# Kernel optimization log

Hardware: AMD Instinct MI355X
Metric: run time of the kernel (lower is better)

The kernel has to match this reference:

```python
import jax, jax.numpy as jnp
import numpy as np

HIDDEN = 1024
BATCH = 32
SEQ = 2048


def setup_inputs() -> dict:
    key = jax.random.key(0)
    k1, k2, k3, k4 = jax.random.split(key, 4)
    decoder_state = jax.random.normal(k1, (BATCH, HIDDEN), dtype=jnp.float32)
    encoder_outputs = jax.random.normal(k2, (BATCH, SEQ, HIDDEN), dtype=jnp.float32)
    # nn.Linear(hidden, hidden, bias=False): y = x @ W.T; store weight as (out, in)
    W = jax.random.normal(k3, (HIDDEN, HIDDEN), dtype=jnp.float32) / np.sqrt(HIDDEN)
    v = jax.random.normal(k4, (1, HIDDEN), dtype=jnp.float32) / np.sqrt(HIDDEN)
    return {"decoder_state": decoder_state, "encoder_outputs": encoder_outputs, "W": W, "v": v}


def reference(decoder_state, encoder_outputs, W, v):
    # projected encoder states: [b, s, h]
    proj = jnp.einsum('bsh,oh->bso', encoder_outputs, W)
    # additive score: tanh(proj + dec) @ v -> [b, s]
    scores = jnp.einsum('bsh,h->bs', jnp.tanh(proj + decoder_state[:, None, :]), v[0])
    weights = jax.nn.softmax(scores, axis=-1)  # [b, s]
    context = jnp.einsum('bs,bsh->bh', weights, encoder_outputs)  # [b, h]
    return (context, weights)
```

## Files before the change

### kernel.cpp

```cpp
#include <hip/hip_runtime.h>
#include <hip/hip_bf16.h>
#include <math.h>

#define HIDDEN 1024
#define BATCH 32
#define SEQ 2048
#define MTOT (BATCH * SEQ)
#define N_PLANES 8

#define BM 128
#define BN 256
#define BK 32
#define NKS (HIDDEN / BK)

typedef __attribute__((ext_vector_type(8))) short          bf16x8;
typedef __attribute__((ext_vector_type(8))) unsigned short ushort8;
typedef __attribute__((ext_vector_type(4))) float          f32x4;

#define GLOAD_LDS16(g, l) __builtin_amdgcn_global_load_lds( \
    (const __attribute__((address_space(1))) void*)(g),      \
    (__attribute__((address_space(3))) void*)(l), 16, 0, 0)

#define BARRIER() asm volatile("s_barrier" ::: "memory")
#define WAITL0()  asm volatile("s_waitcnt lgkmcnt(0)" ::: "memory")
#define WAITL6()  asm volatile("s_waitcnt lgkmcnt(6)" ::: "memory")
#define WAITV4()  asm volatile("s_waitcnt vmcnt(4)" ::: "memory")
#define WAITV8()  asm volatile("s_waitcnt vmcnt(8)" ::: "memory")
#define WAITV0()  asm volatile("s_waitcnt vmcnt(0)" ::: "memory")
#define SCHED0()  __builtin_amdgcn_sched_barrier(0)

__device__ __forceinline__ float fast_tanh(float x) {
    float e = __builtin_amdgcn_exp2f(x * 2.8853900817779268f);
    return 1.0f - 2.0f * __builtin_amdgcn_rcpf(1.0f + e);
}

__device__ __forceinline__ ushort8 cvt8(float4 lo, float4 hi) {
    float va[8] = {lo.x, lo.y, lo.z, lo.w, hi.x, hi.y, hi.z, hi.w};
    ushort8 r;
    #pragma unroll
    for (int j = 0; j < 8; ++j) {
        unsigned u = __float_as_uint(va[j]);
        r[j] = (unsigned short)((u + 0x7FFFu + ((u >> 16) & 1u)) >> 16);
    }
    return r;
}

__global__ __launch_bounds__(256) void convert_w_k(
    const float* __restrict__ W, unsigned short* __restrict__ Wb)
{
    const int i = blockIdx.x * blockDim.x + threadIdx.x;
    float4 a = ((const float4*)W)[(size_t)i * 2];
    float4 b = ((const float4*)W)[(size_t)i * 2 + 1];
    *(ushort8*)&Wb[(size_t)i * 8] = cvt8(a, b);
}

template <bool PARTIALS>
__global__ __launch_bounds__(256, 2) void score_gemm_mfma(
    const float* __restrict__ enc,
    const unsigned short* __restrict__ Wb,
    const float* __restrict__ dec,
    const float* __restrict__ v,
    float* __restrict__ outp)
{
    __shared__ unsigned short As[3][BM][BK];
    __shared__ unsigned short Bs[3][BN][BK];

    const int bid  = blockIdx.x;
    const int xcd  = bid & 7;
    const int slot = bid >> 3;
    const int mt   = xcd * 64 + (slot >> 2);
    const int nt   = slot & 3;
    const int m0   = mt * BM;
    const int n0   = nt * BN;

    const int tid  = threadIdx.x;
    const int wid  = tid >> 6;
    const int lane = tid & 63;
    const int wm   = (wid >> 1) * 64;
    const int wn   = (wid & 1) * 128;

    const int rowb = (lane & 15) * 64;
    const int swzb = (((lane >> 4) ^ (lane & 3)) * 16);

    const int chA0  = wid * 64 + lane;
    const int chA1  = 256 + wid * 64 + lane;
    const int rowA0 = chA0 >> 2, rowA1 = chA1 >> 2;
    const float* encA0 = &enc[(size_t)(m0 + rowA0) * HIDDEN
                              + (((chA0 & 3) ^ (rowA0 & 3)) * 8)];
    const float* encA1 = &enc[(size_t)(m0 + rowA1) * HIDDEN
                              + (((chA1 & 3) ^ (rowA1 & 3)) * 8)];

    auto loadA = [&](int k0, float4& l0, float4& h0, float4& l1, float4& h1) {
        l0 = *(const float4*)(encA0 + k0);
        h0 = *(const float4*)(encA0 + k0 + 4);
        l1 = *(const float4*)(encA1 + k0);
        h1 = *(const float4*)(encA1 + k0 + 4);
    };
    auto writeA = [&](int buf, float4 l0, float4 h0, float4 l1, float4 h1) {
        *(ushort8*)((char*)&As[buf][0][0] + (size_t)chA0 * 16) = cvt8(l0, h0);
        *(ushort8*)((char*)&As[buf][0][0] + (size_t)chA1 * 16) = cvt8(l1, h1);
    };
    auto stageB = [&](int buf, int k0) {
        #pragma unroll
        for (int c = 0; c < 4; ++c) {
            const int chw = c * 256 + wid * 64;
            const int ch  = chw + lane;
            const int row = ch >> 2;
            const int gk  = k0 + (((ch & 3) ^ (row & 3)) * 8);
            GLOAD_LDS16(&Wb[(size_t)(n0 + row) * HIDDEN + gk],
                        (char*)&Bs[buf][0][0] + (size_t)chw * 16);
        }
    };

    {
        float4 p0l0, p0h0, p0l1, p0h1, p1l0, p1h0, p1l1, p1h1;
        loadA(0, p0l0, p0h0, p0l1, p0h1);
        stageB(0, 0);
        loadA(BK, p1l0, p1h0, p1l1, p1h1);
        stageB(1, BK);
        asm volatile("s_waitcnt vmcnt(12)" ::: "memory"); SCHED0();
        writeA(0, p0l0, p0h0, p0l1, p0h1);
        WAITV4(); SCHED0();
        writeA(1, p1l0, p1h0, p1l1, p1h1);
        WAITL0(); SCHED0();
        BARRIER();
    }

    f32x4 acc[4][8] = {};
    float4 al0, ah0, al1, ah1;

    #pragma unroll 1
    for (int t = 0; t < NKS; ++t) {
        const int cur  = t % 3;
        const int nxt  = (t + 2) % 3;
        const int prv  = (t + 1) % 3;
        const bool more = (t + 2 < NKS);
        const int knxt = (t + 2) * BK;
        const char* Ab = (const char*)&As[cur][0][0];
        const char* Bb = (const char*)&Bs[cur][0][0];

        bf16x8 af[4], bf[8];

        #pragma unroll
        for (int fi = 0; fi < 4; ++fi)
            af[fi] = *(const bf16x8*)(Ab + (wm + fi * 16) * 64 + rowb + swzb);
        #pragma unroll
        for (int fj = 0; fj < 8; ++fj)
            bf[fj] = *(const bf16x8*)(Bb + (wn + fj * 16) * 64 + rowb + swzb);
        SCHED0();

        if (t >= 1 && t + 1 < NKS) {
            WAITV4(); SCHED0();
            writeA(prv, al0, ah0, al1, ah1);
            SCHED0();
        }
        if (more) {
            loadA(knxt, al0, ah0, al1, ah1);
            SCHED0();
            stageB(nxt, knxt);
            SCHED0();
        }

        WAITL6(); SCHED0();
        __builtin_amdgcn_s_setprio(1);
        #pragma unroll
        for (int fi = 0; fi < 4; ++fi)
            #pragma unroll
            for (int fj = 0; fj < 4; ++fj)
                acc[fi][fj] = __builtin_amdgcn_mfma_f32_16x16x32_bf16(
                    af[fi], bf[fj], acc[fi][fj], 0, 0, 0);
        __builtin_amdgcn_s_setprio(0);
        SCHED0();

        WAITL0(); SCHED0();
        __builtin_amdgcn_s_setprio(1);
        #pragma unroll
        for (int fi = 0; fi < 4; ++fi)
            #pragma unroll
            for (int fj = 4; fj < 8; ++fj)
                acc[fi][fj] = __builtin_amdgcn_mfma_f32_16x16x32_bf16(
                    af[fi], bf[fj], acc[fi][fj], 0, 0, 0);
        __builtin_amdgcn_s_setprio(0);
        SCHED0();

        if (more)             { WAITV8(); }
        else if (t + 1 < NKS) { WAITV0(); }
        SCHED0();
        if (t + 1 < NKS) BARRIER();
    }

    const int rowgrp = lane >> 4;
    const int col    = lane & 15;
    const int b      = m0 >> 11;
    const float* decb = dec + (size_t)b * HIDDEN;

    float2 dv[8];
    #pragma unroll
    for (int fj = 0; fj < 8; ++fj) {
        const int n = n0 + wn + fj * 16 + col;
        dv[fj] = make_float2(decb[n], v[n]);
    }

    const size_t plane = (size_t)(nt * 2 + (wid & 1)) * MTOT;

    #pragma unroll
    for (int fi = 0; fi < 4; ++fi) {
        #pragma unroll
        for (int r = 0; r < 4; ++r) {
            const int m = m0 + wm + fi * 16 + rowgrp * 4 + r;
            float rp = 0.f;
            #pragma unroll
            for (int fj = 0; fj < 8; ++fj)
                rp = fmaf(fast_tanh(acc[fi][fj][r] + dv[fj].x), dv[fj].y, rp);
            rp += __shfl_xor(rp, 1, 64);
            rp += __shfl_xor(rp, 2, 64);
            rp += __shfl_xor(rp, 4, 64);
            rp += __shfl_xor(rp, 8, 64);
            if (col == 0) {
                if (PARTIALS) outp[plane + m] = rp;
                else          atomicAdd(&outp[m], rp);
            }
        }
    }
}

template <bool PARTIALS>
__global__ __launch_bounds__(256) void softmax_k(
    const float* __restrict__ scores, float* __restrict__ wts)
{
    __shared__ float redmax[4];
    __shared__ float redsum[4];
    const int b = blockIdx.x;
    const int tid = threadIdx.x;

    float vals[8];
    float lmax = -1e30f;
    #pragma unroll
    for (int j = 0; j < 8; ++j) {
        const int idx = b * SEQ + tid + j * 256;
        float s;
        if (PARTIALS) {
            s = 0.f;
            #pragma unroll
            for (int p = 0; p < N_PLANES; ++p)
                s += scores[(size_t)p * MTOT + idx];
        } else {
            s = scores[idx];
        }
        vals[j] = s;
        lmax = fmaxf(lmax, s);
    }
    #pragma unroll
    for (int off = 1; off < 64; off <<= 1)
        lmax = fmaxf(lmax, __shfl_xor(lmax, off, 64));
    if ((tid & 63) == 0) redmax[tid >> 6] = lmax;
    __syncthreads();
    const float gmax = fmaxf(fmaxf(redmax[0], redmax[1]),
                             fmaxf(redmax[2], redmax[3]));

    float lsum = 0.f;
    #pragma unroll
    for (int j = 0; j < 8; ++j) {
        vals[j] = expf(vals[j] - gmax);
        lsum += vals[j];
    }
    #pragma unroll
    for (int off = 1; off < 64; off <<= 1)
        lsum += __shfl_xor(lsum, off, 64);
    if ((tid & 63) == 0) redsum[tid >> 6] = lsum;
    __syncthreads();
    const float inv = 1.f / (redsum[0] + redsum[1] + redsum[2] + redsum[3]);

    #pragma unroll
    for (int j = 0; j < 8; ++j)
        wts[b * SEQ + tid + j * 256] = vals[j] * inv;
}

__global__ __launch_bounds__(256) void context_f32_k(
    const float* __restrict__ enc,
    const float* __restrict__ w,
    float* __restrict__ ctx)
{
    const int b     = blockIdx.x >> 3;
    const int chunk = blockIdx.x & 7;
    const int sOff  = threadIdx.x >> 5;
    const int quad  = threadIdx.x & 31;
    const int h     = chunk * 128 + quad * 4;

    float4 acc = {0.f, 0.f, 0.f, 0.f};
    #pragma unroll 4
    for (int s = sOff; s < SEQ; s += 8) {
        const float ws = w[b * SEQ + s];
        const float4 e = *(const float4*)&enc[(size_t)(b * SEQ + s) * HIDDEN + h];
        acc.x = fmaf(ws, e.x, acc.x);
        acc.y = fmaf(ws, e.y, acc.y);
        acc.z = fmaf(ws, e.z, acc.z);
        acc.w = fmaf(ws, e.w, acc.w);
    }

    __shared__ float4 red[8][32];
    red[sOff][quad] = acc;
    __syncthreads();
    if (sOff == 0) {
        float4 r = red[0][quad];
        #pragma unroll
        for (int t = 1; t < 8; ++t) {
            r.x += red[t][quad].x; r.y += red[t][quad].y;
            r.z += red[t][quad].z; r.w += red[t][quad].w;
        }
        *(float4*)&ctx[b * HIDDEN + h] = r;
    }
}

__global__ __launch_bounds__(256) void score_gemm_f32(
    const float* __restrict__ enc, const float* __restrict__ W,
    const float* __restrict__ dec, const float* __restrict__ v,
    float* __restrict__ scores)
{
    __shared__ float As[16][64 + 1];
    __shared__ float Bs[16][64 + 1];
    const int tid = threadIdx.x;
    const int m0 = (blockIdx.x >> 4) * 64;
    const int n0 = (blockIdx.x & 15) * 64;
    const int ty = tid >> 4, tx = tid & 15;
    const int lr = tid >> 2, lc = tid & 3;
    float acc[4][4] = {};
    for (int k0 = 0; k0 < HIDDEN; k0 += 16) {
        float4 a = *(const float4*)&enc[(size_t)(m0 + lr) * HIDDEN + k0 + lc * 4];
        float4 b = *(const float4*)&W  [(size_t)(n0 + lr) * HIDDEN + k0 + lc * 4];
        __syncthreads();
        As[lc*4+0][lr]=a.x; As[lc*4+1][lr]=a.y; As[lc*4+2][lr]=a.z; As[lc*4+3][lr]=a.w;
        Bs[lc*4+0][lr]=b.x; Bs[lc*4+1][lr]=b.y; Bs[lc*4+2][lr]=b.z; Bs[lc*4+3][lr]=b.w;
        __syncthreads();
        #pragma unroll
        for (int k = 0; k < 16; ++k) {
            float4 av = *(const float4*)&As[k][ty * 4];
            float4 bv = *(const float4*)&Bs[k][tx * 4];
            float aa[4] = {av.x, av.y, av.z, av.w};
            float bb[4] = {bv.x, bv.y, bv.z, bv.w};
            #pragma unroll
            for (int i = 0; i < 4; ++i)
                #pragma unroll
                for (int j = 0; j < 4; ++j)
                    acc[i][j] = fmaf(aa[i], bb[j], acc[i][j]);
        }
    }
    float rowpart[4];
    #pragma unroll
    for (int i = 0; i < 4; ++i) {
        const int m = m0 + ty * 4 + i;
        const int b = m >> 11;
        float rp = 0.f;
        #pragma unroll
        for (int j = 0; j < 4; ++j) {
            const int n = n0 + tx * 4 + j;
            rp = fmaf(fast_tanh(acc[i][j] + dec[b * HIDDEN + n]), v[n], rp);
        }
        rowpart[i] = rp;
    }
    #pragma unroll
    for (int off = 1; off <= 8; off <<= 1)
        #pragma unroll
        for (int i = 0; i < 4; ++i)
            rowpart[i] += __shfl_xor(rowpart[i], off, 64);
    if (tx == 0)
        #pragma unroll
        for (int i = 0; i < 4; ++i)
            atomicAdd(&scores[m0 + ty * 4 + i], rowpart[i]);
}

extern "C" void kernel_launch(void* const* d_in, const int* in_sizes, int n_in,
                              void* d_out, int out_size, void* d_ws, size_t ws_size,
                              hipStream_t stream) {
    const float* dec = (const float*)d_in[0];
    const float* enc = (const float*)d_in[1];
    const float* W   = (const float*)d_in[2];
    const float* v   = (const float*)d_in[3];

    float* out = (float*)d_out;
    float* ctx = out;
    float* wts = out + BATCH * HIDDEN;

    const size_t part_bytes   = (size_t)N_PLANES * MTOT * sizeof(float);
    const size_t wb_bytes     = (size_t)HIDDEN * HIDDEN * 2;
    const size_t scores_bytes = (size_t)MTOT * sizeof(float);
    const size_t need = part_bytes + wb_bytes;

    if (ws_size >= need) {
        float* partial       = (float*)d_ws;
        unsigned short* Wb   = (unsigned short*)((char*)d_ws + part_bytes);

        convert_w_k<<<dim3(512), dim3(256), 0, stream>>>(W, Wb);
        score_gemm_mfma<true><<<dim3(2048), dim3(256), 0, stream>>>(enc, Wb, dec, v, partial);
        softmax_k<true><<<dim3(BATCH), dim3(256), 0, stream>>>(partial, wts);
        context_f32_k<<<dim3(BATCH * 8), dim3(256), 0, stream>>>(enc, wts, ctx);
    } else {
        float* scores = (float*)d_ws;
        hipMemsetAsync(scores, 0, scores_bytes, stream);
        score_gemm_f32<<<dim3(16384), dim3(256), 0, stream>>>(enc, W, dec, v, scores);
        softmax_k<false><<<dim3(BATCH), dim3(256), 0, stream>>>(scores, wts);
        context_f32_k<<<dim3(BATCH * 8), dim3(256), 0, stream>>>(enc, wts, ctx);
    }
}
```

Measured before the change: 208.1 us.

## Load encoder A fragments straight to registers, skipping LDS staging

New measurement: 338.2 us. 62.5% more time.

```diff
diff --git a/kernel.cpp b/kernel.cpp
--- a/kernel.cpp
+++ b/kernel.cpp
@@ -21,13 +21,13 @@
     (const __attribute__((address_space(1))) void*)(g),      \
     (__attribute__((address_space(3))) void*)(l), 16, 0, 0)
 
-#define BARRIER() asm volatile("s_barrier" ::: "memory")
-#define WAITL0()  asm volatile("s_waitcnt lgkmcnt(0)" ::: "memory")
-#define WAITL6()  asm volatile("s_waitcnt lgkmcnt(6)" ::: "memory")
-#define WAITV4()  asm volatile("s_waitcnt vmcnt(4)" ::: "memory")
-#define WAITV8()  asm volatile("s_waitcnt vmcnt(8)" ::: "memory")
-#define WAITV0()  asm volatile("s_waitcnt vmcnt(0)" ::: "memory")
-#define SCHED0()  __builtin_amdgcn_sched_barrier(0)
+#define BARRIER()  asm volatile("s_barrier" ::: "memory")
+#define WAITL0()   asm volatile("s_waitcnt lgkmcnt(0)" ::: "memory")
+#define WAITV0()   asm volatile("s_waitcnt vmcnt(0)" ::: "memory")
+#define WAITV4()   asm volatile("s_waitcnt vmcnt(4)" ::: "memory")
+#define WAITV8()   asm volatile("s_waitcnt vmcnt(8)" ::: "memory")
+#define WAITV12()  asm volatile("s_waitcnt vmcnt(12)" ::: "memory")
+#define SCHED0()   __builtin_amdgcn_sched_barrier(0)
 
 __device__ __forceinline__ float fast_tanh(float x) {
     float e = __builtin_amdgcn_exp2f(x * 2.8853900817779268f);
@@ -62,7 +62,6 @@
     const float* __restrict__ v,
     float* __restrict__ outp)
 {
-    __shared__ unsigned short As[3][BM][BK];
     __shared__ unsigned short Bs[3][BN][BK];
 
     const int bid  = blockIdx.x;
@@ -82,24 +81,21 @@
     const int rowb = (lane & 15) * 64;
     const int swzb = (((lane >> 4) ^ (lane & 3)) * 16);
 
-    const int chA0  = wid * 64 + lane;
-    const int chA1  = 256 + wid * 64 + lane;
-    const int rowA0 = chA0 >> 2, rowA1 = chA1 >> 2;
-    const float* encA0 = &enc[(size_t)(m0 + rowA0) * HIDDEN
-                              + (((chA0 & 3) ^ (rowA0 & 3)) * 8)];
-    const float* encA1 = &enc[(size_t)(m0 + rowA1) * HIDDEN
-                              + (((chA1 & 3) ^ (rowA1 & 3)) * 8)];
-
-    auto loadA = [&](int k0, float4& l0, float4& h0, float4& l1, float4& h1) {
-        l0 = *(const float4*)(encA0 + k0);
-        h0 = *(const float4*)(encA0 + k0 + 4);
-        l1 = *(const float4*)(encA1 + k0);
-        h1 = *(const float4*)(encA1 + k0 + 4);
+    const float* encA[4];
+    #pragma unroll
+    for (int fi = 0; fi < 4; ++fi)
+        encA[fi] = enc + (size_t)(m0 + wm + fi * 16 + (lane & 15)) * HIDDEN
+                       + (lane >> 4) * 8;
+
+    float4 aA[8];
+    auto loadA = [&](int k0) {
+        #pragma unroll
+        for (int fi = 0; fi < 4; ++fi) {
+            aA[2 * fi]     = *(const float4*)(encA[fi] + k0);
+            aA[2 * fi + 1] = *(const float4*)(encA[fi] + k0 + 4);
+        }
     };
-    auto writeA = [&](int buf, float4 l0, float4 h0, float4 l1, float4 h1) {
-        *(ushort8*)((char*)&As[buf][0][0] + (size_t)chA0 * 16) = cvt8(l0, h0);
-        *(ushort8*)((char*)&As[buf][0][0] + (size_t)chA1 * 16) = cvt8(l1, h1);
-    };
+
     auto stageB = [&](int buf, int k0) {
         #pragma unroll
         for (int c = 0; c < 4; ++c) {
@@ -112,56 +108,40 @@
         }
     };
 
-    {
-        float4 p0l0, p0h0, p0l1, p0h1, p1l0, p1h0, p1l1, p1h1;
-        loadA(0, p0l0, p0h0, p0l1, p0h1);
-        stageB(0, 0);
-        loadA(BK, p1l0, p1h0, p1l1, p1h1);
-        stageB(1, BK);
-        asm volatile("s_waitcnt vmcnt(12)" ::: "memory"); SCHED0();
-        writeA(0, p0l0, p0h0, p0l1, p0h1);
-        WAITV4(); SCHED0();
-        writeA(1, p1l0, p1h0, p1l1, p1h1);
-        WAITL0(); SCHED0();
-        BARRIER();
-    }
+    stageB(0, 0);
+    loadA(0);
+    stageB(1, BK);
+    WAITV12(); SCHED0();
+    BARRIER();
 
     f32x4 acc[4][8] = {};
-    float4 al0, ah0, al1, ah1;
+    bf16x8 af[4];
 
     #pragma unroll 1
     for (int t = 0; t < NKS; ++t) {
         const int cur  = t % 3;
         const int nxt  = (t + 2) % 3;
-        const int prv  = (t + 1) % 3;
         const bool more = (t + 2 < NKS);
-        const int knxt = (t + 2) * BK;
-        const char* Ab = (const char*)&As[cur][0][0];
         const char* Bb = (const char*)&Bs[cur][0][0];
 
-        bf16x8 af[4], bf[8];
-
+        bf16x8 bf[4];
+
+        #pragma unroll
+        for (int fj = 0; fj < 4; ++fj)
+            bf[fj] = *(const bf16x8*)(Bb + (wn + fj * 16) * 64 + rowb + swzb);
+        SCHED0();
+
+        if (t + 1 < NKS) { WAITV4(); } else { WAITV0(); }
+        SCHED0();
         #pragma unroll
         for (int fi = 0; fi < 4; ++fi)
-            af[fi] = *(const bf16x8*)(Ab + (wm + fi * 16) * 64 + rowb + swzb);
-        #pragma unroll
-        for (int fj = 0; fj < 8; ++fj)
-            bf[fj] = *(const bf16x8*)(Bb + (wn + fj * 16) * 64 + rowb + swzb);
-        SCHED0();
-
-        if (t >= 1 && t + 1 < NKS) {
-            WAITV4(); SCHED0();
-            writeA(prv, al0, ah0, al1, ah1);
-            SCHED0();
-        }
-        if (more) {
-            loadA(knxt, al0, ah0, al1, ah1);
-            SCHED0();
-            stageB(nxt, knxt);
-            SCHED0();
-        }
-
-        WAITL6(); SCHED0();
+            af[fi] = __builtin_bit_cast(bf16x8, cvt8(aA[2 * fi], aA[2 * fi + 1]));
+        SCHED0();
+
+        if (t + 1 < NKS) { loadA((t + 1) * BK); SCHED0(); }
+        if (more)        { stageB(nxt, (t + 2) * BK); SCHED0(); }
+
+        WAITL0(); SCHED0();
         __builtin_amdgcn_s_setprio(1);
         #pragma unroll
         for (int fi = 0; fi < 4; ++fi)
@@ -172,19 +152,22 @@
         __builtin_amdgcn_s_setprio(0);
         SCHED0();
 
+        #pragma unroll
+        for (int fj = 0; fj < 4; ++fj)
+            bf[fj] = *(const bf16x8*)(Bb + (wn + (fj + 4) * 16) * 64 + rowb + swzb);
         WAITL0(); SCHED0();
         __builtin_amdgcn_s_setprio(1);
         #pragma unroll
         for (int fi = 0; fi < 4; ++fi)
             #pragma unroll
-            for (int fj = 4; fj < 8; ++fj)
-                acc[fi][fj] = __builtin_amdgcn_mfma_f32_16x16x32_bf16(
-                    af[fi], bf[fj], acc[fi][fj], 0, 0, 0);
+            for (int fj = 0; fj < 4; ++fj)
+                acc[fi][fj + 4] = __builtin_amdgcn_mfma_f32_16x16x32_bf16(
+                    af[fi], bf[fj], acc[fi][fj + 4], 0, 0, 0);
         __builtin_amdgcn_s_setprio(0);
         SCHED0();
 
-        if (more)             { WAITV8(); }
-        else if (t + 1 < NKS) { WAITV0(); }
+        if (more)             { WAITV12(); }
+        else if (t + 1 < NKS) { WAITV8(); }
         SCHED0();
         if (t + 1 < NKS) BARRIER();
     }
@@ -396,7 +379,7 @@
         context_f32_k<<<dim3(BATCH * 8), dim3(256), 0, stream>>>(enc, wts, ctx);
     } else {
         float* scores = (float*)d_ws;
-        hipMemsetAsync(scores, 0, scores_bytes, stream);
+        (void)hipMemsetAsync(scores, 0, scores_bytes, stream);
         score_gemm_f32<<<dim3(16384), dim3(256), 0, stream>>>(enc, W, dec, v, scores);
         softmax_k<false><<<dim3(BATCH), dim3(256), 0, stream>>>(scores, wts);
         context_f32_k<<<dim3(BATCH * 8), dim3(256), 0, stream>>>(enc, wts, ctx);
```

## Emit bf16 copy of encoder in score GEMM and use it for context

Applied to the files above, without the earlier changes.

Result: slower. 295.9 us (+42.2%).

```diff
diff --git a/kernel.cpp b/kernel.cpp
--- a/kernel.cpp
+++ b/kernel.cpp
@@ -26,6 +26,7 @@
 #define WAITL6()  asm volatile("s_waitcnt lgkmcnt(6)" ::: "memory")
 #define WAITV4()  asm volatile("s_waitcnt vmcnt(4)" ::: "memory")
 #define WAITV8()  asm volatile("s_waitcnt vmcnt(8)" ::: "memory")
+#define WAITV12() asm volatile("s_waitcnt vmcnt(12)" ::: "memory")
 #define WAITV0()  asm volatile("s_waitcnt vmcnt(0)" ::: "memory")
 #define SCHED0()  __builtin_amdgcn_sched_barrier(0)
 
@@ -54,13 +55,14 @@
     *(ushort8*)&Wb[(size_t)i * 8] = cvt8(a, b);
 }
 
-template <bool PARTIALS>
+template <bool WRITEB>
 __global__ __launch_bounds__(256, 2) void score_gemm_mfma(
     const float* __restrict__ enc,
     const unsigned short* __restrict__ Wb,
     const float* __restrict__ dec,
     const float* __restrict__ v,
-    float* __restrict__ outp)
+    float* __restrict__ outp,
+    unsigned short* __restrict__ encb)
 {
     __shared__ unsigned short As[3][BM][BK];
     __shared__ unsigned short Bs[3][BN][BK];
@@ -85,10 +87,14 @@
     const int chA0  = wid * 64 + lane;
     const int chA1  = 256 + wid * 64 + lane;
     const int rowA0 = chA0 >> 2, rowA1 = chA1 >> 2;
-    const float* encA0 = &enc[(size_t)(m0 + rowA0) * HIDDEN
-                              + (((chA0 & 3) ^ (rowA0 & 3)) * 8)];
-    const float* encA1 = &enc[(size_t)(m0 + rowA1) * HIDDEN
-                              + (((chA1 & 3) ^ (rowA1 & 3)) * 8)];
+    const int swA0  = ((chA0 & 3) ^ (rowA0 & 3)) * 8;
+    const int swA1  = ((chA1 & 3) ^ (rowA1 & 3)) * 8;
+    const float* encA0 = &enc[(size_t)(m0 + rowA0) * HIDDEN + swA0];
+    const float* encA1 = &enc[(size_t)(m0 + rowA1) * HIDDEN + swA1];
+    unsigned short* encbA0 =
+        WRITEB ? &encb[(size_t)(m0 + rowA0) * HIDDEN + swA0] : nullptr;
+    unsigned short* encbA1 =
+        WRITEB ? &encb[(size_t)(m0 + rowA1) * HIDDEN + swA1] : nullptr;
 
     auto loadA = [&](int k0, float4& l0, float4& h0, float4& l1, float4& h1) {
         l0 = *(const float4*)(encA0 + k0);
@@ -96,9 +102,18 @@
         l1 = *(const float4*)(encA1 + k0);
         h1 = *(const float4*)(encA1 + k0 + 4);
     };
-    auto writeA = [&](int buf, float4 l0, float4 h0, float4 l1, float4 h1) {
-        *(ushort8*)((char*)&As[buf][0][0] + (size_t)chA0 * 16) = cvt8(l0, h0);
-        *(ushort8*)((char*)&As[buf][0][0] + (size_t)chA1 * 16) = cvt8(l1, h1);
+    auto writeA = [&](int buf, int k0,
+                      float4 l0, float4 h0, float4 l1, float4 h1) {
+        ushort8 r0 = cvt8(l0, h0);
+        ushort8 r1 = cvt8(l1, h1);
+        *(ushort8*)((char*)&As[buf][0][0] + (size_t)chA0 * 16) = r0;
+        *(ushort8*)((char*)&As[buf][0][0] + (size_t)chA1 * 16) = r1;
+        if constexpr (WRITEB) {
+            if (nt == 0) {
+                *(ushort8*)(encbA0 + k0) = r0;
+                *(ushort8*)(encbA1 + k0) = r1;
+            }
+        }
     };
     auto stageB = [&](int buf, int k0) {
         #pragma unroll
@@ -118,10 +133,10 @@
         stageB(0, 0);
         loadA(BK, p1l0, p1h0, p1l1, p1h1);
         stageB(1, BK);
-        asm volatile("s_waitcnt vmcnt(12)" ::: "memory"); SCHED0();
-        writeA(0, p0l0, p0h0, p0l1, p0h1);
+        WAITV12(); SCHED0();
+        writeA(0, 0, p0l0, p0h0, p0l1, p0h1);
         WAITV4(); SCHED0();
-        writeA(1, p1l0, p1h0, p1l1, p1h1);
+        writeA(1, BK, p1l0, p1h0, p1l1, p1h1);
         WAITL0(); SCHED0();
         BARRIER();
     }
@@ -151,7 +166,7 @@
 
         if (t >= 1 && t + 1 < NKS) {
             WAITV4(); SCHED0();
-            writeA(prv, al0, ah0, al1, ah1);
+            writeA(prv, (t + 1) * BK, al0, ah0, al1, ah1);
             SCHED0();
         }
         if (more) {
@@ -183,7 +198,7 @@
         __builtin_amdgcn_s_setprio(0);
         SCHED0();
 
-        if (more)             { WAITV8(); }
+        if (more)             { WAITV12(); }
         else if (t + 1 < NKS) { WAITV0(); }
         SCHED0();
         if (t + 1 < NKS) BARRIER();
@@ -216,10 +231,7 @@
             rp += __shfl_xor(rp, 2, 64);
             rp += __shfl_xor(rp, 4, 64);
             rp += __shfl_xor(rp, 8, 64);
-            if (col == 0) {
-                if (PARTIALS) outp[plane + m] = rp;
-                else          atomicAdd(&outp[m], rp);
-            }
+            if (col == 0) outp[plane + m] = rp;
         }
     }
 }
@@ -274,6 +286,37 @@
     #pragma unroll
     for (int j = 0; j < 8; ++j)
         wts[b * SEQ + tid + j * 256] = vals[j] * inv;
+}
+
+__global__ __launch_bounds__(256) void context_bf16_k(
+    const unsigned short* __restrict__ encb,
+    const float* __restrict__ w,
+    float* __restrict__ ctx)
+{
+    const int b     = blockIdx.x >> 3;
+    const int chunk = blockIdx.x & 7;
+    const int sOff  = threadIdx.x >> 4;
+    const int hg    = threadIdx.x & 15;
+    const int h     = chunk * 128 + hg * 8;
+
+    float acc[8] = {};
+    for (int s = sOff; s < SEQ; s += 16) {
+        const float ws = w[b * SEQ + s];
+        ushort8 e = *(const ushort8*)&encb[(size_t)(b * SEQ + s) * HIDDEN + h];
+        #pragma unroll
+        for (int j = 0; j < 8; ++j)
+            acc[j] = fmaf(ws, __uint_as_float((unsigned)e[j] << 16), acc[j]);
+    }
+    __shared__ float red[16][128];
+    #pragma unroll
+    for (int j = 0; j < 8; ++j) red[sOff][hg * 8 + j] = acc[j];
+    __syncthreads();
+    if (threadIdx.x < 128) {
+        float r = 0.f;
+        #pragma unroll
+        for (int g = 0; g < 16; ++g) r += red[g][threadIdx.x];
+        ctx[b * HIDDEN + chunk * 128 + threadIdx.x] = r;
+    }
 }
 
 __global__ __launch_bounds__(256) void context_f32_k(
@@ -383,20 +426,35 @@
 
     const size_t part_bytes   = (size_t)N_PLANES * MTOT * sizeof(float);
     const size_t wb_bytes     = (size_t)HIDDEN * HIDDEN * 2;
+    const size_t encb_bytes   = (size_t)MTOT * HIDDEN * 2;
     const size_t scores_bytes = (size_t)MTOT * sizeof(float);
-    const size_t need = part_bytes + wb_bytes;
-
-    if (ws_size >= need) {
-        float* partial       = (float*)d_ws;
-        unsigned short* Wb   = (unsigned short*)((char*)d_ws + part_bytes);
+
+    const size_t need_full = part_bytes + wb_bytes + encb_bytes;
+    const size_t need_mid  = part_bytes + wb_bytes;
+
+    if (ws_size >= need_full) {
+        float* partial     = (float*)d_ws;
+        unsigned short* Wb = (unsigned short*)((char*)d_ws + part_bytes);
+        unsigned short* encb =
+            (unsigned short*)((char*)d_ws + part_bytes + wb_bytes);
 
         convert_w_k<<<dim3(512), dim3(256), 0, stream>>>(W, Wb);
-        score_gemm_mfma<true><<<dim3(2048), dim3(256), 0, stream>>>(enc, Wb, dec, v, partial);
+        score_gemm_mfma<true><<<dim3(2048), dim3(256), 0, stream>>>(
+            enc, Wb, dec, v, partial, encb);
+        softmax_k<true><<<dim3(BATCH), dim3(256), 0, stream>>>(partial, wts);
+        context_bf16_k<<<dim3(BATCH * 8), dim3(256), 0, stream>>>(encb, wts, ctx);
+    } else if (ws_size >= need_mid) {
+        float* partial     = (float*)d_ws;
+        unsigned short* Wb = (unsigned short*)((char*)d_ws + part_bytes);
+
+        convert_w_k<<<dim3(512), dim3(256), 0, stream>>>(W, Wb);
+        score_gemm_mfma<false><<<dim3(2048), dim3(256), 0, stream>>>(
+            enc, Wb, dec, v, partial, nullptr);
         softmax_k<true><<<dim3(BATCH), dim3(256), 0, stream>>>(partial, wts);
         context_f32_k<<<dim3(BATCH * 8), dim3(256), 0, stream>>>(enc, wts, ctx);
     } else {
         float* scores = (float*)d_ws;
-        hipMemsetAsync(scores, 0, scores_bytes, stream);
+        (void)hipMemsetAsync(scores, 0, scores_bytes, stream);
         score_gemm_f32<<<dim3(16384), dim3(256), 0, stream>>>(enc, W, dec, v, scores);
         softmax_k<false><<<dim3(BATCH), dim3(256), 0, stream>>>(scores, wts);
         context_f32_k<<<dim3(BATCH * 8), dim3(256), 0, stream>>>(enc, wts, ctx);
```
